# Optimization experiments

Measured on AMD Instinct MI355X. Metric: run time of the kernel, lower is better.

Reference implementation:

```python
import jax, jax.numpy as jnp
import numpy as np

N_BITS = 8
QMAX = float(2 ** (N_BITS - 1) - 1)   # 127
QMIN = -QMAX - 1.0                     # -128
EPS = 1e-8


def _fq(x, scale):
    # symmetric fake quant: round, clamp, dequant
    return jnp.clip(jnp.round(x / scale), QMIN, QMAX) * scale


def fake_quant_per_token(x):
    # one scale per [..., :] vector (amax over last dim)
    max_abs = jnp.max(jnp.abs(x), axis=-1, keepdims=True)
    scale = jnp.maximum(max_abs / QMAX, EPS)
    return _fq(x, scale)


def fake_quant_per_channel(w):
    # w: [out, in]; ch_axis=0 -> one scale per output row (reduce over dim 1)
    max_abs = jnp.max(jnp.abs(w), axis=1, keepdims=True)
    scale = jnp.maximum(max_abs / QMAX, EPS)
    return _fq(w, scale)


def setup_inputs() -> dict:
    key = jax.random.key(0)
    kx, kw, kb = jax.random.split(key, 3)
    B, S, D_IN, D_OUT = 4, 2048, 4096, 4096
    x = jax.random.normal(kx, (B, S, D_IN), dtype=jnp.float32)
    w = jax.random.normal(kw, (D_OUT, D_IN), dtype=jnp.float32) * 0.02
    b = jax.random.normal(kb, (D_OUT,), dtype=jnp.float32) * 0.02
    return {"x": x, "w": w, "b": b}


def reference(x, w, b):
    # fake-quant path: W8 per-channel weight, A8 per-token activation
    w_q = fake_quant_per_channel(w)           # [O, I]
    x_q = fake_quant_per_token(x)             # [B, S, I]
    y = jnp.einsum('bsi,oi->bso', x_q, w_q) + b
    return y
```

## Files before the change

### kernel.cpp

```cpp
#include <hip/hip_runtime.h>
#include <hip/hip_bf16.h>


#define K_DIM 4096
#define N_DIM 4096
#define NT (K_DIM / 128)

typedef int v4i __attribute__((ext_vector_type(4)));

__device__ __forceinline__ void cp16(void* lds, const void* g) {
    __builtin_amdgcn_global_load_lds(
        (const __attribute__((address_space(1))) void*)g,
        (__attribute__((address_space(3))) void*)lds, 16, 0, 0);
}

__global__ __launch_bounds__(256) void quant_rows_kernel(
    const float* __restrict__ x, const float* __restrict__ w, int M,
    char* __restrict__ qx, char* __restrict__ qw,
    float* __restrict__ sx, float* __restrict__ sw) {
    const int blk = blockIdx.x;
    const bool is_x = blk < M;
    const int row = is_x ? blk : blk - M;
    const float* rp = (is_x ? x : w) + (size_t)row * 4096;
    char* qdst = is_x ? qx : qw;
    float* sdst = is_x ? sx : sw;

    const int tid = threadIdx.x;

    float4 v[4];
#pragma unroll
    for (int i = 0; i < 4; ++i)
        v[i] = *(const float4*)(rp + 4 * (tid + 256 * i));

    float m = 0.0f;
#pragma unroll
    for (int i = 0; i < 4; ++i) {
        m = fmaxf(m, fmaxf(fmaxf(fabsf(v[i].x), fabsf(v[i].y)),
                           fmaxf(fabsf(v[i].z), fabsf(v[i].w))));
    }
#pragma unroll
    for (int off = 32; off > 0; off >>= 1)
        m = fmaxf(m, __shfl_down(m, off));

    __shared__ float red[4];
    if ((tid & 63) == 0) red[tid >> 6] = m;
    __syncthreads();
    const float amax = fmaxf(fmaxf(red[0], red[1]), fmaxf(red[2], red[3]));
    const float scale = fmaxf(amax / 127.0f, 1e-8f);
    const float qs = 1.0f / scale;

    int* qout = (int*)(qdst + (size_t)row * 4096);
#pragma unroll
    for (int i = 0; i < 4; ++i) {
        int q0 = (int)fminf(fmaxf(rintf(v[i].x * qs), -128.0f), 127.0f);
        int q1 = (int)fminf(fmaxf(rintf(v[i].y * qs), -128.0f), 127.0f);
        int q2 = (int)fminf(fmaxf(rintf(v[i].z * qs), -128.0f), 127.0f);
        int q3 = (int)fminf(fmaxf(rintf(v[i].w * qs), -128.0f), 127.0f);
        qout[tid + 256 * i] =
            (q0 & 255) | ((q1 & 255) << 8) | ((q2 & 255) << 16) | ((q3 & 255) << 24);
    }
    if (tid == 0) sdst[row] = scale;
}

__global__ __launch_bounds__(512, 2) void gemm_i8_kernel(
    const char* __restrict__ qx, const char* __restrict__ qw,
    const float* __restrict__ sx, const float* __restrict__ sw,
    const float* __restrict__ bias, float* __restrict__ y) {

    __shared__ __align__(16) char lds[131072];

    const int tid  = threadIdx.x;
    const int wave = tid >> 6;
    const int lane = tid & 63;
    const int ln   = lane & 15;
    const int lg   = lane >> 4;
    const int wm   = wave >> 2;
    const int wn   = wave & 3;
    const int ksf  = (wave >> 2) & 1;

    const int bm = blockIdx.y;
    const int bn = blockIdx.x;

    const int ci0 = tid,       r0s = ci0 >> 3, c0s = (ci0 & 7) ^ (r0s & 7);
    const int ci1 = tid + 512, r1s = ci1 >> 3, c1s = (ci1 & 7) ^ (r1s & 7);
    const char* aS0 = qx + (size_t)(bm * 256 + r0s) * K_DIM + c0s * 16;
    const char* aS1 = qx + (size_t)(bm * 256 + r1s) * K_DIM + c1s * 16;
    const char* bS0 = qw + (size_t)(bn * 256 + r0s) * K_DIM + c0s * 16;
    const char* bS1 = qw + (size_t)(bn * 256 + r1s) * K_DIM + c1s * 16;
    const int ldsC0 = ci0 * 16, ldsC1 = ci1 * 16;

#define SLOT_A(par, h) ((par) * 65536 + (h) * 16384)
#define SLOT_B(par, h) ((par) * 65536 + 32768 + (h) * 16384)
#define STAGE_A(par, h, t) do {                                              \
    cp16(lds + SLOT_A(par, h) + ldsC0,                                       \
         aS0 + (size_t)(h) * 128 * K_DIM + (size_t)(t) * 128);               \
    cp16(lds + SLOT_A(par, h) + ldsC1,                                       \
         aS1 + (size_t)(h) * 128 * K_DIM + (size_t)(t) * 128); } while (0)
#define STAGE_B(par, h, t) do {                                              \
    cp16(lds + SLOT_B(par, h) + ldsC0,                                       \
         bS0 + (size_t)(h) * 128 * K_DIM + (size_t)(t) * 128);               \
    cp16(lds + SLOT_B(par, h) + ldsC1,                                       \
         bS1 + (size_t)(h) * 128 * K_DIM + (size_t)(t) * 128); } while (0)

#define BAR()   __builtin_amdgcn_s_barrier()
#define FENCE() asm volatile("" ::: "memory")

    const int ch0 = (lg ^ (ln & 7)) * 16;
    const int aRd = wm * 16384 + ln * 128;
    const int bRd = 32768 + wn * 8192 + ln * 128;

    v4i acc[8][4] = {};

    STAGE_A(0, 0, 0); STAGE_A(0, 1, 0);
    STAGE_B(0, 0, 0); STAGE_B(0, 1, 0);
    asm volatile("s_waitcnt vmcnt(0)" ::: "memory");
    BAR(); FENCE();

    for (int t = 0; t < NT; ++t) {
        const int par  = t & 1;
        const int base = par << 16;

        if (t + 1 < NT) {
            STAGE_A(par ^ 1, 0, t + 1); STAGE_A(par ^ 1, 1, t + 1);
            STAGE_B(par ^ 1, 0, t + 1); STAGE_B(par ^ 1, 1, t + 1);
        }

#pragma unroll
        for (int ks2 = 0; ks2 < 2; ++ks2) {
            const int ch = ch0 ^ (((ks2 ^ ksf) & 1) << 6);
            v4i afr[8], bfr[4];
#pragma unroll
            for (int m = 0; m < 8; ++m)
                afr[m] = *(const v4i*)(lds + base + aRd + m * 2048 + ch);
#pragma unroll
            for (int n = 0; n < 4; ++n)
                bfr[n] = *(const v4i*)(lds + base + bRd + n * 2048 + ch);
            __builtin_amdgcn_s_setprio(1);
#pragma unroll
            for (int m = 0; m < 8; ++m)
#pragma unroll
                for (int n = 0; n < 4; ++n)
                    acc[m][n] = __builtin_amdgcn_mfma_i32_16x16x64_i8(
                        afr[m], bfr[n], acc[m][n], 0, 0, 0);
            __builtin_amdgcn_s_setprio(0);
        }

        asm volatile("s_waitcnt vmcnt(0)" ::: "memory");
        BAR(); FENCE();
    }

    const int m_base = bm * 256 + wm * 128;
    const int n_base = bn * 256 + wn * 64;

    float sxr[8][4];
#pragma unroll
    for (int m = 0; m < 8; ++m)
#pragma unroll
        for (int r = 0; r < 4; ++r)
            sxr[m][r] = sx[m_base + m * 16 + lg * 4 + r];

#pragma unroll
    for (int n = 0; n < 4; ++n) {
        const int col = n_base + n * 16 + ln;
        const float swv = sw[col];
        const float bv  = bias[col];
#pragma unroll
        for (int m = 0; m < 8; ++m) {
            const int row = m_base + m * 16 + lg * 4;
#pragma unroll
            for (int r = 0; r < 4; ++r) {
                y[(size_t)(row + r) * N_DIM + col] =
                    (float)acc[m][n][r] * sxr[m][r] * swv + bv;
            }
        }
    }
#undef SLOT_A
#undef SLOT_B
#undef STAGE_A
#undef STAGE_B
#undef BAR
#undef FENCE
}

extern "C" void kernel_launch(void* const* d_in, const int* in_sizes, int n_in,
                              void* d_out, int out_size, void* d_ws, size_t ws_size,
                              hipStream_t stream) {
    const float* x = (const float*)d_in[0];
    const float* w = (const float*)d_in[1];
    const float* b = (const float*)d_in[2];
    float* y = (float*)d_out;

    const int M = in_sizes[0] / K_DIM;
    const int O = in_sizes[1] / K_DIM;

    char* qx = (char*)d_ws;
    char* qw = qx + (size_t)M * K_DIM;
    float* sx = (float*)(qw + (size_t)O * K_DIM);
    float* sw = sx + M;

    quant_rows_kernel<<<M + O, 256, 0, stream>>>(x, w, M, qx, qw, sx, sw);

    dim3 grid(N_DIM / 256, M / 256);
    gemm_i8_kernel<<<grid, 512, 0, stream>>>(qx, qw, sx, sw, b, y);
}
```

Before: 384.5 us.

## Shrink GEMM block tile to 128x256 with K-step 64 and 4 waves

The int8 GEMM block tile changes from 256x256 with 8 waves and K-step 128 to 128x256 with 4 waves and K-step 64. LDS per block drops from 128KB to 48KB, with a new XOR swizzle for 64-byte rows. Each wave still computes a 128x64 output tile. The aim is more resident blocks per CU and twice as many blocks across the grid, at the cost of less A/B reuse per block, twice as many barriers per K, and more global traffic.

```diff
diff --git a/kernel.cpp b/kernel.cpp
--- a/kernel.cpp
+++ b/kernel.cpp
@@ -4,7 +4,7 @@
 
 #define K_DIM 4096
 #define N_DIM 4096
-#define NT (K_DIM / 128)
+#define NT (K_DIM / 64)
 
 typedef int v4i __attribute__((ext_vector_type(4)));
 
@@ -62,94 +62,94 @@
     if (tid == 0) sdst[row] = scale;
 }
 
-__global__ __launch_bounds__(512, 2) void gemm_i8_kernel(
+__global__ __launch_bounds__(256, 2) void gemm_i8_kernel(
     const char* __restrict__ qx, const char* __restrict__ qw,
     const float* __restrict__ sx, const float* __restrict__ sw,
     const float* __restrict__ bias, float* __restrict__ y) {
 
-    __shared__ __align__(16) char lds[131072];
+    __shared__ __align__(16) char lds[49152];
 
     const int tid  = threadIdx.x;
     const int wave = tid >> 6;
     const int lane = tid & 63;
     const int ln   = lane & 15;
     const int lg   = lane >> 4;
-    const int wm   = wave >> 2;
-    const int wn   = wave & 3;
-    const int ksf  = (wave >> 2) & 1;
+    const int wn   = wave;
 
     const int bm = blockIdx.y;
     const int bn = blockIdx.x;
 
-    const int ci0 = tid,       r0s = ci0 >> 3, c0s = (ci0 & 7) ^ (r0s & 7);
-    const int ci1 = tid + 512, r1s = ci1 >> 3, c1s = (ci1 & 7) ^ (r1s & 7);
-    const char* aS0 = qx + (size_t)(bm * 256 + r0s) * K_DIM + c0s * 16;
-    const char* aS1 = qx + (size_t)(bm * 256 + r1s) * K_DIM + c1s * 16;
-    const char* bS0 = qw + (size_t)(bn * 256 + r0s) * K_DIM + c0s * 16;
-    const char* bS1 = qw + (size_t)(bn * 256 + r1s) * K_DIM + c1s * 16;
-    const int ldsC0 = ci0 * 16, ldsC1 = ci1 * 16;
-
-#define SLOT_A(par, h) ((par) * 65536 + (h) * 16384)
-#define SLOT_B(par, h) ((par) * 65536 + 32768 + (h) * 16384)
-#define STAGE_A(par, h, t) do {                                              \
-    cp16(lds + SLOT_A(par, h) + ldsC0,                                       \
-         aS0 + (size_t)(h) * 128 * K_DIM + (size_t)(t) * 128);               \
-    cp16(lds + SLOT_A(par, h) + ldsC1,                                       \
-         aS1 + (size_t)(h) * 128 * K_DIM + (size_t)(t) * 128); } while (0)
-#define STAGE_B(par, h, t) do {                                              \
-    cp16(lds + SLOT_B(par, h) + ldsC0,                                       \
-         bS0 + (size_t)(h) * 128 * K_DIM + (size_t)(t) * 128);               \
-    cp16(lds + SLOT_B(par, h) + ldsC1,                                       \
-         bS1 + (size_t)(h) * 128 * K_DIM + (size_t)(t) * 128); } while (0)
+    const char* aSrc[2]; int aDst[2];
+#pragma unroll
+    for (int j = 0; j < 2; ++j) {
+        const int ci = tid + 256 * j, row = ci >> 2, pos = ci & 3;
+        const int sc = pos ^ ((row >> 1) & 3);
+        aSrc[j] = qx + (size_t)(bm * 128 + row) * K_DIM + sc * 16;
+        aDst[j] = ci * 16;
+    }
+    const char* bSrc[4]; int bDst[4];
+#pragma unroll
+    for (int j = 0; j < 4; ++j) {
+        const int ci = tid + 256 * j, row = ci >> 2, pos = ci & 3;
+        const int sc = pos ^ ((row >> 1) & 3);
+        bSrc[j] = qw + (size_t)(bn * 256 + row) * K_DIM + sc * 16;
+        bDst[j] = 8192 + ci * 16;
+    }
+
+#define PAR_SZ 24576
+#define STAGE(par, t) do {                                                   \
+    _Pragma("unroll")                                                        \
+    for (int j = 0; j < 2; ++j)                                              \
+        cp16(lds + (par) * PAR_SZ + aDst[j], aSrc[j] + (size_t)(t) * 64);    \
+    _Pragma("unroll")                                                        \
+    for (int j = 0; j < 4; ++j)                                              \
+        cp16(lds + (par) * PAR_SZ + bDst[j], bSrc[j] + (size_t)(t) * 64);    \
+    } while (0)
 
 #define BAR()   __builtin_amdgcn_s_barrier()
 #define FENCE() asm volatile("" ::: "memory")
 
-    const int ch0 = (lg ^ (ln & 7)) * 16;
-    const int aRd = wm * 16384 + ln * 128;
-    const int bRd = 32768 + wn * 8192 + ln * 128;
+    const int chByte = (lg ^ ((ln >> 1) & 3)) * 16;
+    int aOff[8], bOff[4];
+#pragma unroll
+    for (int mt = 0; mt < 8; ++mt) aOff[mt] = (mt * 16 + ln) * 64 + chByte;
+#pragma unroll
+    for (int nt = 0; nt < 4; ++nt)
+        bOff[nt] = 8192 + (wn * 64 + nt * 16 + ln) * 64 + chByte;
 
     v4i acc[8][4] = {};
 
-    STAGE_A(0, 0, 0); STAGE_A(0, 1, 0);
-    STAGE_B(0, 0, 0); STAGE_B(0, 1, 0);
+    STAGE(0, 0);
     asm volatile("s_waitcnt vmcnt(0)" ::: "memory");
     BAR(); FENCE();
 
     for (int t = 0; t < NT; ++t) {
         const int par  = t & 1;
-        const int base = par << 16;
-
-        if (t + 1 < NT) {
-            STAGE_A(par ^ 1, 0, t + 1); STAGE_A(par ^ 1, 1, t + 1);
-            STAGE_B(par ^ 1, 0, t + 1); STAGE_B(par ^ 1, 1, t + 1);
-        }
-
-#pragma unroll
-        for (int ks2 = 0; ks2 < 2; ++ks2) {
-            const int ch = ch0 ^ (((ks2 ^ ksf) & 1) << 6);
-            v4i afr[8], bfr[4];
-#pragma unroll
-            for (int m = 0; m < 8; ++m)
-                afr[m] = *(const v4i*)(lds + base + aRd + m * 2048 + ch);
+        const int base = par * PAR_SZ;
+
+        if (t + 1 < NT) STAGE(par ^ 1, t + 1);
+
+        v4i afr[8], bfr[4];
+#pragma unroll
+        for (int m = 0; m < 8; ++m)
+            afr[m] = *(const v4i*)(lds + base + aOff[m]);
+#pragma unroll
+        for (int n = 0; n < 4; ++n)
+            bfr[n] = *(const v4i*)(lds + base + bOff[n]);
+        __builtin_amdgcn_s_setprio(1);
+#pragma unroll
+        for (int m = 0; m < 8; ++m)
 #pragma unroll
             for (int n = 0; n < 4; ++n)
-                bfr[n] = *(const v4i*)(lds + base + bRd + n * 2048 + ch);
-            __builtin_amdgcn_s_setprio(1);
-#pragma unroll
-            for (int m = 0; m < 8; ++m)
-#pragma unroll
-                for (int n = 0; n < 4; ++n)
-                    acc[m][n] = __builtin_amdgcn_mfma_i32_16x16x64_i8(
-                        afr[m], bfr[n], acc[m][n], 0, 0, 0);
-            __builtin_amdgcn_s_setprio(0);
-        }
+                acc[m][n] = __builtin_amdgcn_mfma_i32_16x16x64_i8(
+                    afr[m], bfr[n], acc[m][n], 0, 0, 0);
+        __builtin_amdgcn_s_setprio(0);
 
         asm volatile("s_waitcnt vmcnt(0)" ::: "memory");
         BAR(); FENCE();
     }
 
-    const int m_base = bm * 256 + wm * 128;
+    const int m_base = bm * 128;
     const int n_base = bn * 256 + wn * 64;
 
     float sxr[8][4];
@@ -174,10 +174,8 @@
             }
         }
     }
-#undef SLOT_A
-#undef SLOT_B
-#undef STAGE_A
-#undef STAGE_B
+#undef PAR_SZ
+#undef STAGE
 #undef BAR
 #undef FENCE
 }
@@ -200,6 +198,6 @@
 
     quant_rows_kernel<<<M + O, 256, 0, stream>>>(x, w, M, qx, qw, sx, sw);
 
-    dim3 grid(N_DIM / 256, M / 256);
-    gemm_i8_kernel<<<grid, 512, 0, stream>>>(qx, qw, sx, sw, b, y);
-}
+    dim3 grid(N_DIM / 256, M / 128);
+    gemm_i8_kernel<<<grid, 256, 0, stream>>>(qx, qw, sx, sw, b, y);
+}
```

Result: slower. 405.7 us (+5.5%).
